# Kernel optimization log

Hardware: AMD Instinct MI355X
Metric: run time of the kernel (lower is better)

The kernel has to match this reference:

```python
import jax, jax.numpy as jnp
import numpy as np

N_NODES = 100_000
N_EDGES = 1_600_000
N_TRI = 1_000_000
HID = 64
NNZ0 = 2 * N_EDGES  # d0: 2 nonzeros per edge
NNZ1 = 3 * N_TRI    # d1: 3 nonzeros per 2-clique


def spmm(rows, cols, vals, x, n_out):
    """out[r] = sum_{k: rows[k]==r} vals[k] * x[cols[k]]  (sparse @ dense)."""
    return jax.ops.segment_sum(vals[:, None] * x[cols], rows, num_segments=n_out)


def setup_inputs() -> dict:
    key = jax.random.key(0)
    ks = jax.random.split(key, 12)
    q = jax.random.normal(ks[0], (N_NODES, HID), dtype=jnp.float32)
    p = jax.random.normal(ks[1], (N_EDGES, HID), dtype=jnp.float32)
    # attention weights used as divisors -> keep bounded away from 0
    A0 = jax.random.uniform(ks[2], (N_NODES,), jnp.float32, 0.5, 1.5)
    A1 = jax.random.uniform(ks[3], (N_EDGES,), jnp.float32, 0.5, 1.5)
    A2 = jax.random.uniform(ks[4], (N_TRI,), jnp.float32, 0.5, 1.5)
    alpha_raw = jnp.ones((1,), dtype=jnp.float32)
    d0_rows = jax.random.randint(ks[5], (NNZ0,), 0, N_EDGES, dtype=jnp.int32)
    d0_cols = jax.random.randint(ks[6], (NNZ0,), 0, N_NODES, dtype=jnp.int32)
    d0_vals = jax.random.normal(ks[7], (NNZ0,), dtype=jnp.float32)
    d1_rows = jax.random.randint(ks[8], (NNZ1,), 0, N_TRI, dtype=jnp.int32)
    d1_cols = jax.random.randint(ks[9], (NNZ1,), 0, N_EDGES, dtype=jnp.int32)
    d1_vals = jax.random.normal(ks[10], (NNZ1,), dtype=jnp.float32)
    return {
        "q": q, "p": p, "A0": A0, "A1": A1, "A2": A2, "alpha_raw": alpha_raw,
        "d0_rows": d0_rows, "d0_cols": d0_cols, "d0_vals": d0_vals,
        "d1_rows": d1_rows, "d1_cols": d1_cols, "d1_vals": d1_vals,
    }


def reference(q, p, A0, A1, A2, alpha_raw,
              d0_rows, d0_cols, d0_vals, d1_rows, d1_cols, d1_vals):
    n_nodes = q.shape[0]
    n_edges = p.shape[0]
    n_tri = A2.shape[0]
    alpha = jax.nn.sigmoid(alpha_raw)  # opt['alpha_multiplier']
    a0 = A0[:, None]  # [N,1]
    a1 = A1[:, None]  # [E,1]
    a2 = A2[:, None]  # [T,1]

    # bracket == 'gradient'
    # qPart = -alpha * d0^T (A1 * d0 (q / A0)) / A0
    d0ainvq = spmm(d0_rows, d0_cols, d0_vals, q / a0, n_edges)          # [E,H]
    qPart = -alpha * spmm(d0_cols, d0_rows, d0_vals, a1 * d0ainvq, n_nodes) / a0

    # pPart = -alpha * ( d1^T (A2 * d1 (p / A1)) / A1 + d0 (d0^T p / A0) )
    d1ainvp = spmm(d1_rows, d1_cols, d1_vals, p / a1, n_tri)            # [T,H]
    d1ad1Part = spmm(d1_cols, d1_rows, d1_vals, a2 * d1ainvp, n_edges) / a1
    a0invd0tp = spmm(d0_cols, d0_rows, d0_vals, p, n_nodes) / a0        # [N,H]
    d0d0aPart = spmm(d0_rows, d0_cols, d0_vals, a0invd0tp, n_edges)     # [E,H]
    pPart = -alpha * (d1ad1Part + d0d0aPart)

    return (qPart, pPart)
```

## Files before the change

kernel.cpp:

```cpp
#include <hip/hip_runtime.h>

#define HID 64

typedef unsigned short ushort_t;
typedef unsigned int uint_t;
typedef unsigned char uchar_t;
typedef unsigned long long ull_t;
typedef float fx4 __attribute__((ext_vector_type(4)));

__device__ __forceinline__ ushort_t f2bf(float f) {
    uint_t u = __float_as_uint(f);
    u += 0x7FFFu + ((u >> 16) & 1u);
    return (ushort_t)(u >> 16);
}
__device__ __forceinline__ float bf2f(ushort_t h) {
    return __uint_as_float(((uint_t)h) << 16);
}

__device__ __forceinline__ void ntstore4(float* dst, float a, float b, float c, float d) {
    fx4 t; t[0] = a; t[1] = b; t[2] = c; t[3] = d;
    __builtin_nontemporal_store(t, (fx4*)dst);
}

__device__ __forceinline__ int shard_of(int row, uint_t scale) {
    return (int)(((ull_t)(uint_t)row * scale) >> 32);
}


__global__ __launch_bounds__(256) void count_rank8(
    const int* __restrict__ d0r, const int* __restrict__ d0c,
    const int* __restrict__ d1r, const int* __restrict__ d1c,
    int* __restrict__ rowcat,
    uchar_t* __restrict__ rkA0, uchar_t* __restrict__ rkB0,
    uchar_t* __restrict__ rkA1, uchar_t* __restrict__ rkB1,
    int off_d0r, int off_d0c, int off_d1r, int off_d1c,
    int nnz0, int nnz1)
{
    int b = blockIdx.x;
    int cb0 = (nnz0 + 255) >> 8;
    if (b < cb0) {
        int k = b * 256 + threadIdx.x;
        if (k < nnz0) {
            int A = d0r[k], B = d0c[k];
            int r0 = atomicAdd(&rowcat[off_d0r + A + 1], 1);
            int r1 = atomicAdd(&rowcat[off_d0c + B + 1], 1);
            rkA0[k] = (uchar_t)r0;
            rkB0[k] = (uchar_t)r1;
        }
    } else {
        int k = (b - cb0) * 256 + threadIdx.x;
        if (k < nnz1) {
            int A = d1r[k], B = d1c[k];
            int r0 = atomicAdd(&rowcat[off_d1r + A + 1], 1);
            int r1 = atomicAdd(&rowcat[off_d1c + B + 1], 1);
            rkA1[k] = (uchar_t)r0;
            rkB1[k] = (uchar_t)r1;
        }
    }
}

__global__ __launch_bounds__(256) void fill_conv8(
    const int* __restrict__ d0r, const int* __restrict__ d0c,
    const float* __restrict__ v0, const float* __restrict__ A0d,
    const int* __restrict__ d1r, const int* __restrict__ d1c,
    const float* __restrict__ v1, const float* __restrict__ A1d,
    const int* __restrict__ S,
    const uchar_t* __restrict__ rkA0, const uchar_t* __restrict__ rkB0,
    const uchar_t* __restrict__ rkA1, const uchar_t* __restrict__ rkB1,
    int2* __restrict__ pcv,
    int off_d0r, int off_d0c, int off_d1r, int off_d1c,
    uint_t scE, uint_t scN, uint_t scT,
    int nnz0, int nnz1, int npair, int nchunks,
    const float* __restrict__ p, ushort_t* __restrict__ ph, long long np)
{
    int b = blockIdx.x;
    int shard = b & 7;
    int chunk = -1, vb = -1;
    int lim = 9 * npair;
    if (b < lim) {
        int g = b / 9, pos = b - g * 9;
        if (pos == 8) vb = g; else chunk = g;
    } else {
        int rem = b - lim;
        int fleft = (nchunks - npair) * 8;
        if (rem < fleft) chunk = npair + (rem >> 3);
        else vb = npair + (rem - fleft);
    }
    if (chunk >= 0) {
        int cb0 = (nnz0 + 255) >> 8;
        if (chunk < cb0) {
            int k = chunk * 256 + threadIdx.x;
            if (k < nnz0) {
                int A = d0r[k];
                int B = d0c[k];
                if (shard_of(A, scE) == shard) {
                    float v = v0[k];
                    int2 e; e.x = B; e.y = __float_as_int(v / A0d[B]);
                    pcv[S[off_d0r + A] + rkA0[k]] = e;
                }
                if (shard_of(B, scN) == shard) {
                    float v = v0[k];
                    int2 e; e.x = A; e.y = __float_as_int(v);
                    pcv[S[off_d0c + B] + rkB0[k]] = e;
                }
            }
        } else {
            int k = (chunk - cb0) * 256 + threadIdx.x;
            if (k < nnz1) {
                int A = d1r[k];
                int B = d1c[k];
                if (shard_of(A, scT) == shard) {
                    float v = v1[k];
                    int2 e; e.x = B; e.y = __float_as_int(v / A1d[B]);
                    pcv[S[off_d1r + A] + rkA1[k]] = e;
                }
                if (shard_of(B, scE) == shard) {
                    float v = v1[k];
                    int2 e; e.x = A; e.y = __float_as_int(v);
                    pcv[S[off_d1c + B] + rkB1[k]] = e;
                }
            }
        }
    } else if (vb >= 0) {
        const fx4* p4 = (const fx4*)p;
        ushort4* h4p = (ushort4*)ph;
        long long nf4 = np >> 2;
        long long f0 = (long long)vb * 1024 + threadIdx.x;
#pragma unroll
        for (int c = 0; c < 4; ++c) {
            long long f = f0 + c * 256;
            if (f < nf4) {
                fx4 v = __builtin_nontemporal_load(p4 + f);
                ushort4 o;
                o.x = f2bf(v[0]); o.y = f2bf(v[1]); o.z = f2bf(v[2]); o.w = f2bf(v[3]);
                h4p[f] = o;
            }
        }
    }
}

#define SCAN_TPB 256
#define SCAN_IPT 32
#define SCAN_TILE (SCAN_TPB * SCAN_IPT)

__global__ __launch_bounds__(256) void scan1(int* __restrict__ data,
                                             int* __restrict__ blockSums, int n) {
    __shared__ int sdata[SCAN_TPB];
    int base = blockIdx.x * SCAN_TILE + threadIdx.x * SCAN_IPT;
    int v[SCAN_IPT];
    int s = 0;
#pragma unroll
    for (int i = 0; i < SCAN_IPT; ++i) {
        int idx = base + i;
        int x = (idx < n) ? data[idx] : 0;
        s += x;
        v[i] = s;
    }
    sdata[threadIdx.x] = s;
    __syncthreads();
    for (int off = 1; off < SCAN_TPB; off <<= 1) {
        int t = (threadIdx.x >= off) ? sdata[threadIdx.x - off] : 0;
        __syncthreads();
        sdata[threadIdx.x] += t;
        __syncthreads();
    }
    int excl = (threadIdx.x == 0) ? 0 : sdata[threadIdx.x - 1];
#pragma unroll
    for (int i = 0; i < SCAN_IPT; ++i) {
        int idx = base + i;
        if (idx < n) data[idx] = v[i] + excl;
    }
    if (threadIdx.x == SCAN_TPB - 1) blockSums[blockIdx.x] = sdata[SCAN_TPB - 1];
}

__global__ __launch_bounds__(1024) void scan2(int* __restrict__ blockSums, int nb) {
    __shared__ int sdata[1024];
    int x = (threadIdx.x < nb) ? blockSums[threadIdx.x] : 0;
    sdata[threadIdx.x] = x;
    __syncthreads();
    for (int off = 1; off < 1024; off <<= 1) {
        int t = (threadIdx.x >= off) ? sdata[threadIdx.x - off] : 0;
        __syncthreads();
        sdata[threadIdx.x] += t;
        __syncthreads();
    }
    if (threadIdx.x < nb) blockSums[threadIdx.x] = sdata[threadIdx.x];
}

__global__ __launch_bounds__(256) void scan3(int* __restrict__ data,
                                             const int* __restrict__ blockSums, int n) {
    if (blockIdx.x == 0) return;
    int add = blockSums[blockIdx.x - 1];
    int base = blockIdx.x * SCAN_TILE + threadIdx.x;
#pragma unroll
    for (int i = 0; i < SCAN_IPT; ++i) {
        int idx = base + i * SCAN_TPB;
        if (idx < n) data[idx] += add;
    }
}


template <int SRCH>
__device__ __forceinline__ float4 gather_row(const void* __restrict__ xv, int col, int h4) {
    if constexpr (SRCH) {
        ushort4 hv = *((const ushort4*)((const ushort_t*)xv + (size_t)col * HID) + h4);
        float4 r; r.x = bf2f(hv.x); r.y = bf2f(hv.y); r.z = bf2f(hv.z); r.w = bf2f(hv.w);
        return r;
    } else {
        return *((const float4*)((const float*)xv + (size_t)col * HID) + h4);
    }
}

template <int SRCH, int OUTH>
__device__ __forceinline__ void spmm4_body(
    const int* __restrict__ rps, const int2* __restrict__ pcv,
    const void* __restrict__ xv, void* __restrict__ outv,
    const float* __restrict__ rmul, const float* __restrict__ rdiv,
    const float* __restrict__ alpha_raw, int nrows, int blk)
{
    int h4 = threadIdx.x & 15;
    int sub16 = threadIdx.x >> 4;
    int rbase = (blk * 16 + sub16) * 4;
    if (rbase >= nrows) return;
    int rp[5];
#pragma unroll
    for (int i = 0; i < 5; ++i) rp[i] = rps[min(rbase + i, nrows)];
    int len[4], last[4];
#pragma unroll
    for (int r = 0; r < 4; ++r) {
        len[r] = rp[r + 1] - rp[r];
        last[r] = max(rp[r + 1] - 1, 0);
    }
    int maxlen = max(max(len[0], len[1]), max(len[2], len[3]));
    float4 acc[4];
#pragma unroll
    for (int r = 0; r < 4; ++r) acc[r] = float4{0.f, 0.f, 0.f, 0.f};

    for (int j = 0; j < maxlen; j += 2) {
        int2 e0[4], e1[4];
#pragma unroll
        for (int r = 0; r < 4; ++r) {
            e0[r] = pcv[min(rp[r] + j, last[r])];
            e1[r] = pcv[min(rp[r] + j + 1, last[r])];
        }
        float4 g0[4], g1[4];
#pragma unroll
        for (int r = 0; r < 4; ++r) g0[r] = gather_row<SRCH>(xv, e0[r].x, h4);
#pragma unroll
        for (int r = 0; r < 4; ++r) g1[r] = gather_row<SRCH>(xv, e1[r].x, h4);
#pragma unroll
        for (int r = 0; r < 4; ++r) {
            float va = (j < len[r]) ? __int_as_float(e0[r].y) : 0.f;
            float vb = (j + 1 < len[r]) ? __int_as_float(e1[r].y) : 0.f;
            acc[r].x += va * g0[r].x + vb * g1[r].x;
            acc[r].y += va * g0[r].y + vb * g1[r].y;
            acc[r].z += va * g0[r].z + vb * g1[r].z;
            acc[r].w += va * g0[r].w + vb * g1[r].w;
        }
    }

    float sgn = alpha_raw ? -(1.0f / (1.0f + expf(-alpha_raw[0]))) : 1.0f;
#pragma unroll
    for (int r = 0; r < 4; ++r) {
        int row = rbase + r;
        if (row >= nrows) break;
        float s = sgn;
        if (rmul) s *= rmul[row];
        if (rdiv) s /= rdiv[row];
        float4 a = acc[r];
        a.x *= s; a.y *= s; a.z *= s; a.w *= s;
        if constexpr (OUTH) {
            ushort4 o;
            o.x = f2bf(a.x); o.y = f2bf(a.y); o.z = f2bf(a.z); o.w = f2bf(a.w);
            *((ushort4*)((ushort_t*)outv + (size_t)row * HID) + h4) = o;
        } else {
            ntstore4((float*)((float4*)((float*)outv + (size_t)row * HID) + h4),
                     a.x, a.y, a.z, a.w);
        }
    }
}

template <int SRCH, int OUTH>
__global__ __launch_bounds__(256) void csr_spmm4(
    const int* __restrict__ rps, const int2* __restrict__ pcv,
    const void* __restrict__ xv, void* __restrict__ outv,
    const float* __restrict__ rmul, const float* __restrict__ rdiv,
    const float* __restrict__ alpha_raw, int nrows)
{
    spmm4_body<SRCH, OUTH>(rps, pcv, xv, outv, rmul, rdiv, alpha_raw, nrows, blockIdx.x);
}

__global__ __launch_bounds__(256) void csr_spmm_dual(
    const int* __restrict__ rpsT, const int* __restrict__ rpsN,
    const int2* __restrict__ pcv, const ushort_t* __restrict__ ph,
    ushort_t* __restrict__ outT, ushort_t* __restrict__ outN,
    const float* __restrict__ a2, int n_tri, int n_nodes, int triBlocks)
{
    if ((int)blockIdx.x < triBlocks)
        spmm4_body<1, 1>(rpsT, pcv, ph, outT, a2, nullptr, nullptr, n_tri, blockIdx.x);
    else
        spmm4_body<1, 1>(rpsN, pcv, ph, outN, nullptr, nullptr, nullptr, n_nodes,
                         blockIdx.x - triBlocks);
}

__global__ __launch_bounds__(256) void csr_fused_epq(
    const int* __restrict__ rpsA, const int* __restrict__ rpsB,
    const int2* __restrict__ pcv,
    const float* __restrict__ q, const ushort_t* __restrict__ tmpn,
    const ushort_t* __restrict__ tmpt,
    const float* __restrict__ a1d, const float* __restrict__ alpha_raw,
    ushort_t* __restrict__ oute1, float* __restrict__ outp, int nrows)
{
    int h4 = threadIdx.x & 15;
    int sub16 = threadIdx.x >> 4;
    int rbase = (blockIdx.x * 16 + sub16) * 4;
    if (rbase >= nrows) return;

    int rpA[5], rpB[5];
#pragma unroll
    for (int i = 0; i < 5; ++i) {
        int idx = min(rbase + i, nrows);
        rpA[i] = rpsA[idx];
        rpB[i] = rpsB[idx];
    }
    int lA[4], lastA[4], lB[4], lastB[4];
#pragma unroll
    for (int r = 0; r < 4; ++r) {
        lA[r] = rpA[r + 1] - rpA[r]; lastA[r] = max(rpA[r + 1] - 1, 0);
        lB[r] = rpB[r + 1] - rpB[r]; lastB[r] = max(rpB[r + 1] - 1, 0);
    }
    int mA = max(max(lA[0], lA[1]), max(lA[2], lA[3]));
    int mB = max(max(lB[0], lB[1]), max(lB[2], lB[3]));

    float4 accQ[4], accN[4], accT[4];
#pragma unroll
    for (int r = 0; r < 4; ++r) {
        accQ[r] = float4{0.f, 0.f, 0.f, 0.f};
        accN[r] = float4{0.f, 0.f, 0.f, 0.f};
        accT[r] = float4{0.f, 0.f, 0.f, 0.f};
    }

    for (int j = 0; j < mA; ++j) {
        int2 e[4];
#pragma unroll
        for (int r = 0; r < 4; ++r) e[r] = pcv[min(rpA[r] + j, lastA[r])];
        float4 gq[4]; ushort4 gn[4];
#pragma unroll
        for (int r = 0; r < 4; ++r)
            gq[r] = *((const float4*)(q + (size_t)e[r].x * HID) + h4);
#pragma unroll
        for (int r = 0; r < 4; ++r)
            gn[r] = *((const ushort4*)(tmpn + (size_t)e[r].x * HID) + h4);
#pragma unroll
        for (int r = 0; r < 4; ++r) {
            float v = (j < lA[r]) ? __int_as_float(e[r].y) : 0.f;
            accQ[r].x += v * gq[r].x; accQ[r].y += v * gq[r].y;
            accQ[r].z += v * gq[r].z; accQ[r].w += v * gq[r].w;
            accN[r].x += v * bf2f(gn[r].x); accN[r].y += v * bf2f(gn[r].y);
            accN[r].z += v * bf2f(gn[r].z); accN[r].w += v * bf2f(gn[r].w);
        }
    }

    for (int j = 0; j < mB; j += 2) {
        int2 e0[4], e1[4];
#pragma unroll
        for (int r = 0; r < 4; ++r) {
            e0[r] = pcv[min(rpB[r] + j, lastB[r])];
            e1[r] = pcv[min(rpB[r] + j + 1, lastB[r])];
        }
        ushort4 g0[4], g1[4];
#pragma unroll
        for (int r = 0; r < 4; ++r)
            g0[r] = *((const ushort4*)(tmpt + (size_t)e0[r].x * HID) + h4);
#pragma unroll
        for (int r = 0; r < 4; ++r)
            g1[r] = *((const ushort4*)(tmpt + (size_t)e1[r].x * HID) + h4);
#pragma unroll
        for (int r = 0; r < 4; ++r) {
            float va = (j < lB[r]) ? __int_as_float(e0[r].y) : 0.f;
            float vb = (j + 1 < lB[r]) ? __int_as_float(e1[r].y) : 0.f;
            accT[r].x += va * bf2f(g0[r].x) + vb * bf2f(g1[r].x);
            accT[r].y += va * bf2f(g0[r].y) + vb * bf2f(g1[r].y);
            accT[r].z += va * bf2f(g0[r].z) + vb * bf2f(g1[r].z);
            accT[r].w += va * bf2f(g0[r].w) + vb * bf2f(g1[r].w);
        }
    }

    float ns = -(1.0f / (1.0f + expf(-alpha_raw[0])));
#pragma unroll
    for (int r = 0; r < 4; ++r) {
        int row = rbase + r;
        if (row >= nrows) break;
        float a1v = a1d[row];
        ushort4 o;
        o.x = f2bf(accQ[r].x * a1v); o.y = f2bf(accQ[r].y * a1v);
        o.z = f2bf(accQ[r].z * a1v); o.w = f2bf(accQ[r].w * a1v);
        *((ushort4*)(oute1 + (size_t)row * HID) + h4) = o;
        float ia = 1.0f / a1v;
        ntstore4((float*)((float4*)(outp + (size_t)row * HID) + h4),
                 ns * (accN[r].x + accT[r].x * ia),
                 ns * (accN[r].y + accT[r].y * ia),
                 ns * (accN[r].z + accT[r].z * ia),
                 ns * (accN[r].w + accT[r].w * ia));
    }
}


__global__ __launch_bounds__(256) void count_rows(const int* __restrict__ ridx,
                                                  int* __restrict__ rowptr, int nnz) {
    int k = blockIdx.x * 256 + threadIdx.x;
    if (k < nnz) atomicAdd(&rowptr[ridx[k] + 1], 1);
}

__global__ __launch_bounds__(256) void copy_int(const int* __restrict__ src,
                                                int* __restrict__ dst, int n) {
    int i = blockIdx.x * 256 + threadIdx.x;
    if (i < n) dst[i] = src[i];
}

__global__ __launch_bounds__(256) void fill_csr(const int* __restrict__ ridx,
                                                const int* __restrict__ cidx,
                                                const float* __restrict__ vals,
                                                int* __restrict__ cursor,
                                                int2* __restrict__ pcv, int nnz) {
    int k = blockIdx.x * 256 + threadIdx.x;
    if (k >= nnz) return;
    int pos = atomicAdd(&cursor[ridx[k]], 1);
    int2 e;
    e.x = cidx[k];
    e.y = __float_as_int(vals[k]);
    pcv[pos] = e;
}

template <int SRCH, int OUTH>
__global__ __launch_bounds__(256) void csr_spmm_t(
    const int* __restrict__ rowptr, const int2* __restrict__ pcv,
    const void* __restrict__ xv, void* __restrict__ outv,
    const float* __restrict__ gdiag, int gdiv,
    const float* __restrict__ rmul,
    const float* __restrict__ rdiv,
    const float* __restrict__ alpha_raw,
    int nrows)
{
    int lane = threadIdx.x & 63;
    int wave = threadIdx.x >> 6;
    int sub = lane >> 4;
    int h4 = lane & 15;
    int row = blockIdx.x * 16 + wave * 4 + sub;
    if (row >= nrows) return;
    int start = rowptr[row], end = rowptr[row + 1];
    float4 acc = {0.f, 0.f, 0.f, 0.f};
    for (int j = start; j < end; ++j) {
        int2 e = pcv[j];
        int c = e.x;
        float v = __int_as_float(e.y);
        if (gdiag) { float t = gdiag[c]; v = gdiv ? v / t : v * t; }
        float4 xvv = gather_row<SRCH>(xv, c, h4);
        acc.x += v * xvv.x; acc.y += v * xvv.y; acc.z += v * xvv.z; acc.w += v * xvv.w;
    }
    float s = 1.0f;
    if (rmul) s *= rmul[row];
    if (rdiv) s /= rdiv[row];
    if (alpha_raw) s *= -(1.0f / (1.0f + expf(-alpha_raw[0])));
    acc.x *= s; acc.y *= s; acc.z *= s; acc.w *= s;
    if constexpr (OUTH) {
        ushort_t* out = (ushort_t*)outv;
        ushort4 o;
        o.x = f2bf(acc.x); o.y = f2bf(acc.y); o.z = f2bf(acc.z); o.w = f2bf(acc.w);
        *((ushort4*)(out + (size_t)row * HID) + h4) = o;
    } else {
        float* out = (float*)outv;
        *((float4*)(out + (size_t)row * HID) + h4) = acc;
    }
}

template <int BH>
__global__ __launch_bounds__(256) void csr_spmm_fused_t(
    const int* __restrict__ rowptrA, const int2* __restrict__ pcvA, const float* __restrict__ xA,
    const int* __restrict__ rowptrB, const int2* __restrict__ pcvB, const void* __restrict__ xBv,
    const float* __restrict__ a1, const float* __restrict__ alpha_raw,
    float* __restrict__ out, int nrows)
{
    int lane = threadIdx.x & 63;
    int wave = threadIdx.x >> 6;
    int sub = lane >> 4;
    int h4 = lane & 15;
    int row = blockIdx.x * 16 + wave * 4 + sub;
    if (row >= nrows) return;

    float4 accA = {0.f, 0.f, 0.f, 0.f};
    {
        int start = rowptrA[row], end = rowptrA[row + 1];
        for (int j = start; j < end; ++j) {
            int2 e = pcvA[j];
            float v = __int_as_float(e.y);
            const float4 xv = *((const float4*)(xA + (size_t)e.x * HID) + h4);
            accA.x += v * xv.x; accA.y += v * xv.y; accA.z += v * xv.z; accA.w += v * xv.w;
        }
    }
    float4 accB = {0.f, 0.f, 0.f, 0.f};
    {
        int start = rowptrB[row], end = rowptrB[row + 1];
        for (int j = start; j < end; ++j) {
            int2 e = pcvB[j];
            float v = __int_as_float(e.y);
            float4 xv = gather_row<BH>(xBv, e.x, h4);
            accB.x += v * xv.x; accB.y += v * xv.y; accB.z += v * xv.z; accB.w += v * xv.w;
        }
    }
    float inv_a1 = 1.0f / a1[row];
    float ns = -(1.0f / (1.0f + expf(-alpha_raw[0])));
    float4 r;
    r.x = ns * (accA.x + accB.x * inv_a1);
    r.y = ns * (accA.y + accB.y * inv_a1);
    r.z = ns * (accA.z + accB.z * inv_a1);
    r.w = ns * (accA.w + accB.w * inv_a1);
    *((float4*)(out + (size_t)row * HID) + h4) = r;
}

__global__ __launch_bounds__(256) void spmm_scatter(
    const int* __restrict__ gidx, const int* __restrict__ sidx,
    const float* __restrict__ vals, const float* __restrict__ x,
    float* __restrict__ out,
    const float* __restrict__ gscale, int ginv,
    const float* __restrict__ sscale, int sinv,
    const float* __restrict__ alpha_raw, int nnz)
{
    int k = (blockIdx.x << 2) | (threadIdx.x >> 6);
    if (k >= nnz) return;
    int h = threadIdx.x & 63;
    int g = gidx[k];
    int s = sidx[k];
    float f = vals[k];
    if (gscale) { float t = gscale[g]; f = ginv ? (f / t) : (f * t); }
    if (sscale) { float t = sscale[s]; f = sinv ? (f / t) : (f * t); }
    if (alpha_raw) {
        float sig = 1.0f / (1.0f + expf(-alpha_raw[0]));
        f = -f * sig;
    }
    atomicAdd(out + (size_t)s * HID + h, f * x[(size_t)g * HID + h]);
}


extern "C" void kernel_launch(void* const* d_in, const int* in_sizes, int n_in,
                              void* d_out, int out_size, void* d_ws, size_t ws_size,
                              hipStream_t stream) {
    const float* q         = (const float*)d_in[0];
    const float* p         = (const float*)d_in[1];
    const float* A0        = (const float*)d_in[2];
    const float* A1        = (const float*)d_in[3];
    const float* A2        = (const float*)d_in[4];
    const float* alpha_raw = (const float*)d_in[5];
    const int*   d0_rows   = (const int*)d_in[6];
    const int*   d0_cols   = (const int*)d_in[7];
    const float* d0_vals   = (const float*)d_in[8];
    const int*   d1_rows   = (const int*)d_in[9];
    const int*   d1_cols   = (const int*)d_in[10];
    const float* d1_vals   = (const float*)d_in[11];

    const int n_nodes = in_sizes[2];
    const int n_edges = in_sizes[3];
    const int n_tri   = in_sizes[4];
    const int nnz0    = in_sizes[6];
    const int nnz1    = in_sizes[9];

    float* qPart = (float*)d_out;
    float* pPart = (float*)d_out + (size_t)n_nodes * HID;

    const size_t qPartBytes = (size_t)n_nodes * HID * sizeof(float);
    const size_t pPartBytes = (size_t)n_edges * HID * sizeof(float);

    dim3 blk(256);

    const int off_d0r = 0;
    const int off_d0c = off_d0r + n_edges;
    const int off_d1r = off_d0c + n_nodes;
    const int off_d1c = off_d1r + n_tri;
    const int NR      = off_d1c + n_edges;

    {
        char* w = (char*)d_ws;
        auto alloc = [&](size_t bytes) -> char* {
            char* ptr = w;
            w += (bytes + 255) & ~(size_t)255;
            return ptr;
        };
        ushort_t* bufA   = (ushort_t*)alloc((size_t)n_edges * HID * sizeof(ushort_t));
        ushort_t* tmp_th = (ushort_t*)alloc((size_t)n_tri * HID * sizeof(ushort_t));
        ushort_t* tmp_nh = (ushort_t*)alloc((size_t)n_nodes * HID * sizeof(ushort_t));
        int*      Z      = (int*)alloc((size_t)(NR + 2) * sizeof(int));
        int*      S      = Z + 1;
        int*      blockSums = (int*)alloc(2048 * sizeof(int));
        int2*     pcvcat = (int2*)alloc(((size_t)nnz0 * 2 + (size_t)nnz1 * 2) * sizeof(int2));
        size_t rankBytes = 2 * ((size_t)nnz0 + (size_t)nnz1);
        uchar_t* rkA0;
        if (rankBytes <= (size_t)n_tri * HID * sizeof(ushort_t))
            rkA0 = (uchar_t*)tmp_th;
        else
            rkA0 = (uchar_t*)alloc(rankBytes);
        uchar_t* rkB0 = rkA0 + nnz0;
        uchar_t* rkA1 = rkB0 + nnz0;
        uchar_t* rkB1 = rkA1 + nnz1;
        size_t needed = (size_t)(w - (char*)d_ws);

        if (needed <= ws_size) {
            hipMemsetAsync(Z, 0, (size_t)(NR + 2) * sizeof(int), stream);
            int cb0 = (nnz0 + 255) / 256;
            int cb1 = (nnz1 + 255) / 256;
            count_rank8<<<cb0 + cb1, blk, 0, stream>>>(
                d0_rows, d0_cols, d1_rows, d1_cols, S,
                rkA0, rkB0, rkA1, rkB1,
                off_d0r, off_d0c, off_d1r, off_d1c, nnz0, nnz1);
            {
                int n = NR + 1;
                int nb = (n + SCAN_TILE - 1) / SCAN_TILE;
                scan1<<<nb, SCAN_TPB, 0, stream>>>(S, blockSums, n);
                scan2<<<1, 1024, 0, stream>>>(blockSums, nb);
                scan3<<<nb, SCAN_TPB, 0, stream>>>(S, blockSums, n);
            }
            long long np = (long long)n_edges * HID;
            int cbc = (int)((np / 4 + 1023) / 1024);
            int nchunks = cb0 + cb1;
            int npair = min(nchunks, cbc);
            int grid = 9 * npair + 8 * (nchunks - npair) + (cbc - npair);
            auto mksc = [](int n) -> uint_t {
                return (uint_t)(((unsigned long long)8 << 32) / (unsigned)n);
            };
            fill_conv8<<<grid, blk, 0, stream>>>(
                d0_rows, d0_cols, d0_vals, A0,
                d1_rows, d1_cols, d1_vals, A1,
                S, rkA0, rkB0, rkA1, rkB1, pcvcat,
                off_d0r, off_d0c, off_d1r, off_d1c,
                mksc(n_edges), mksc(n_nodes), mksc(n_tri),
                nnz0, nnz1, npair, nchunks,
                p, bufA, np);

            int triB  = (n_tri + 63) / 64;
            int nodeB = (n_nodes + 63) / 64;
            int edgeB = (n_edges + 63) / 64;

            csr_spmm_dual<<<triB + nodeB, blk, 0, stream>>>(
                S + off_d1r, S + off_d0c, pcvcat, bufA, tmp_th, tmp_nh,
                A2, n_tri, n_nodes, triB);

            csr_fused_epq<<<edgeB, blk, 0, stream>>>(
                S + off_d0r, S + off_d1c, pcvcat, q, tmp_nh, tmp_th,
                A1, alpha_raw, bufA, pPart, n_edges);

            csr_spmm4<1, 0><<<nodeB, blk, 0, stream>>>(
                S + off_d0c, pcvcat, bufA, qPart, nullptr, A0, alpha_raw, n_nodes);
            return;
        }
    }

    {
        char* w = (char*)d_ws;
        auto alloc = [&](size_t bytes) -> char* {
            char* ptr = w;
            w += (bytes + 255) & ~(size_t)255;
            return ptr;
        };
        float* tmp_t = (float*)alloc((size_t)n_tri * HID * sizeof(float));
        float* tmp_n = (float*)alloc((size_t)n_nodes * HID * sizeof(float));
        size_t rpTotal = (size_t)(n_edges + 1) + (n_nodes + 1) + (n_tri + 1) + (n_edges + 1);
        int* rpBase = (int*)alloc(rpTotal * sizeof(int));
        int* rp_d0r = rpBase;
        int* rp_d0c = rp_d0r + (n_edges + 1);
        int* rp_d1r = rp_d0c + (n_nodes + 1);
        int* rp_d1c = rp_d1r + (n_tri + 1);
        int nmax = n_edges > n_tri ? n_edges : n_tri;
        if (n_nodes > nmax) nmax = n_nodes;
        int* cursor    = (int*)alloc((size_t)nmax * sizeof(int));
        int* blockSums = (int*)alloc(2048 * sizeof(int));
        int2* pcv_d0r = (int2*)alloc((size_t)nnz0 * sizeof(int2));
        int2* pcv_d0c = (int2*)alloc((size_t)nnz0 * sizeof(int2));
        int2* pcv_d1r = (int2*)alloc((size_t)nnz1 * sizeof(int2));
        int2* pcv_d1c = (int2*)alloc((size_t)nnz1 * sizeof(int2));
        size_t needed = (size_t)(w - (char*)d_ws);

        if (needed <= ws_size) {
            hipMemsetAsync(rpBase, 0, rpTotal * sizeof(int), stream);
            dim3 gk0((nnz0 + 255) / 256);
            dim3 gk1((nnz1 + 255) / 256);
            count_rows<<<gk0, blk, 0, stream>>>(d0_rows, rp_d0r, nnz0);
            count_rows<<<gk0, blk, 0, stream>>>(d0_cols, rp_d0c, nnz0);
            count_rows<<<gk1, blk, 0, stream>>>(d1_rows, rp_d1r, nnz1);
            count_rows<<<gk1, blk, 0, stream>>>(d1_cols, rp_d1c, nnz1);

            struct Build {
                int* rowptr; int nout; const int* ridx; const int* cidx; const float* vals;
                int2* pcv; int nnz;
            } builds[4] = {
                { rp_d0r, n_edges, d0_rows, d0_cols, d0_vals, pcv_d0r, nnz0 },
                { rp_d0c, n_nodes, d0_cols, d0_rows, d0_vals, pcv_d0c, nnz0 },
                { rp_d1r, n_tri,   d1_rows, d1_cols, d1_vals, pcv_d1r, nnz1 },
                { rp_d1c, n_edges, d1_cols, d1_rows, d1_vals, pcv_d1c, nnz1 },
            };
            for (int b = 0; b < 4; ++b) {
                int n = builds[b].nout + 1;
                int nb = (n + SCAN_TILE - 1) / SCAN_TILE;
                scan1<<<nb, SCAN_TPB, 0, stream>>>(builds[b].rowptr, blockSums, n);
                scan2<<<1, 1024, 0, stream>>>(blockSums, nb);
                scan3<<<nb, SCAN_TPB, 0, stream>>>(builds[b].rowptr, blockSums, n);
                copy_int<<<(builds[b].nout + 255) / 256, blk, 0, stream>>>(
                    builds[b].rowptr, cursor, builds[b].nout);
                fill_csr<<<(builds[b].nnz + 255) / 256, blk, 0, stream>>>(
                    builds[b].ridx, builds[b].cidx, builds[b].vals, cursor,
                    builds[b].pcv, builds[b].nnz);
            }

            float* tmp_e1 = pPart;
            csr_spmm_t<0, 0><<<(n_edges + 15) / 16, blk, 0, stream>>>(
                rp_d0r, pcv_d0r, q, tmp_e1, A0, 1, A1, nullptr, nullptr, n_edges);
            csr_spmm_t<0, 0><<<(n_nodes + 15) / 16, blk, 0, stream>>>(
                rp_d0c, pcv_d0c, tmp_e1, qPart, nullptr, 0, nullptr, A0, alpha_raw, n_nodes);
            csr_spmm_t<0, 0><<<(n_tri + 15) / 16, blk, 0, stream>>>(
                rp_d1r, pcv_d1r, p, tmp_t, A1, 1, A2, nullptr, nullptr, n_tri);
            csr_spmm_t<0, 0><<<(n_nodes + 15) / 16, blk, 0, stream>>>(
                rp_d0c, pcv_d0c, p, tmp_n, nullptr, 0, nullptr, A0, nullptr, n_nodes);
            csr_spmm_fused_t<0><<<(n_edges + 15) / 16, blk, 0, stream>>>(
                rp_d0r, pcv_d0r, tmp_n,
                rp_d1c, pcv_d1c, tmp_t,
                A1, alpha_raw, pPart, n_edges);
            return;
        }
    }

    {
        float* tmp = (float*)d_ws;
        const size_t triBytes  = (size_t)n_tri * HID * sizeof(float);
        const size_t nodeBytes = qPartBytes;
        dim3 g0((nnz0 + 3) / 4);
        dim3 g1((nnz1 + 3) / 4);
        hipMemsetAsync(qPart, 0, qPartBytes, stream);
        hipMemsetAsync(pPart, 0, pPartBytes, stream);
        spmm_scatter<<<g0, blk, 0, stream>>>(d0_cols, d0_rows, d0_vals, q, pPart,
                                             A0, 1, nullptr, 0, nullptr, nnz0);
        spmm_scatter<<<g0, blk, 0, stream>>>(d0_rows, d0_cols, d0_vals, pPart, qPart,
                                             A1, 0, A0, 1, alpha_raw, nnz0);
        hipMemsetAsync(pPart, 0, pPartBytes, stream);
        hipMemsetAsync(tmp, 0, triBytes, stream);
        spmm_scatter<<<g1, blk, 0, stream>>>(d1_cols, d1_rows, d1_vals, p, tmp,
                                             A1, 1, nullptr, 0, nullptr, nnz1);
        spmm_scatter<<<g1, blk, 0, stream>>>(d1_rows, d1_cols, d1_vals, tmp, pPart,
                                             A2, 0, A1, 1, alpha_raw, nnz1);
        hipMemsetAsync(tmp, 0, nodeBytes, stream);
        spmm_scatter<<<g0, blk, 0, stream>>>(d0_rows, d0_cols, d0_vals, p, tmp,
                                             nullptr, 0, A0, 1, nullptr, nnz0);
        spmm_scatter<<<g0, blk, 0, stream>>>(d0_cols, d0_rows, d0_vals, tmp, pPart,
                                             nullptr, 0, nullptr, 0, alpha_raw, nnz0);
    }
}
```

Before: 1.923 ms.

## Fuse CSR build phases into a single cooperative kernel with grid syncs

```diff
diff --git a/kernel.cpp b/kernel.cpp
--- a/kernel.cpp
+++ b/kernel.cpp
@@ -1,6 +1,11 @@
 #include <hip/hip_runtime.h>
+#include <hip/hip_cooperative_groups.h>
+
+namespace cg = cooperative_groups;
 
 #define HID 64
+#define BT 24
+#define BUILD_BLOCKS 1024
 
 typedef unsigned short ushort_t;
 typedef unsigned int uint_t;
@@ -22,10 +27,169 @@
     __builtin_nontemporal_store(t, (fx4*)dst);
 }
 
+#define SCAN_TPB 256
+#define SCAN_IPT 32
+#define SCAN_TILE (SCAN_TPB * SCAN_IPT)
+
+
+__global__ __launch_bounds__(256, 4) void build_all(
+    const int* __restrict__ d0r, const int* __restrict__ d0c,
+    const float* __restrict__ v0, const float* __restrict__ A0d,
+    const int* __restrict__ d1r, const int* __restrict__ d1c,
+    const float* __restrict__ v1, const float* __restrict__ A1d,
+    int* __restrict__ Z,
+    int* __restrict__ blockSums,
+    int2* __restrict__ pcv,
+    int off_d0r, int off_d0c, int off_d1r, int off_d1c,
+    int nnz0, int nnz1, int NR,
+    const float* __restrict__ p, ushort_t* __restrict__ ph, long long np)
+{
+    cg::grid_group grid = cg::this_grid();
+    const int nth = gridDim.x * 256;
+    const int tid = blockIdx.x * 256 + threadIdx.x;
+    int* S = Z + 1;
+    const int E = nnz0 + nnz1;
+    const fx4* p4 = (const fx4*)p;
+    ushort4* h4p = (ushort4*)ph;
+    const long long nf4 = np >> 2;
+    const long long nf4h = nf4 >> 1;
+
+    for (int i = tid; i < NR + 2; i += nth) Z[i] = 0;
+    __threadfence();
+    grid.sync();
+
+    uint_t rk[BT];
+#pragma unroll
+    for (int i = 0; i < BT; ++i) {
+        int k = tid + i * nth;
+        uint_t r = 0;
+        if (k < nnz0) {
+            int A = d0r[k], B = d0c[k];
+            uint_t ra = (uint_t)atomicAdd(&S[off_d0r + A + 1], 1);
+            uint_t rb = (uint_t)atomicAdd(&S[off_d0c + B + 1], 1);
+            r = (ra << 16) | rb;
+        } else if (k < E) {
+            int kk = k - nnz0;
+            int A = d1r[kk], B = d1c[kk];
+            uint_t ra = (uint_t)atomicAdd(&S[off_d1r + A + 1], 1);
+            uint_t rb = (uint_t)atomicAdd(&S[off_d1c + B + 1], 1);
+            r = (ra << 16) | rb;
+        }
+        rk[i] = r;
+    }
+    for (long long f = tid; f < nf4h; f += nth) {
+        fx4 v = __builtin_nontemporal_load(p4 + f);
+        ushort4 o;
+        o.x = f2bf(v[0]); o.y = f2bf(v[1]); o.z = f2bf(v[2]); o.w = f2bf(v[3]);
+        h4p[f] = o;
+    }
+    __threadfence();
+    grid.sync();
+
+    const int n = NR + 1;
+    const int ntiles = (n + SCAN_TILE - 1) / SCAN_TILE;
+    __shared__ int sdata[SCAN_TPB];
+    if ((int)blockIdx.x < ntiles) {
+        int base = blockIdx.x * SCAN_TILE + threadIdx.x * SCAN_IPT;
+        int v[SCAN_IPT];
+        int s = 0;
+#pragma unroll
+        for (int i = 0; i < SCAN_IPT; ++i) {
+            int idx = base + i;
+            int x = (idx < n) ? S[idx] : 0;
+            s += x;
+            v[i] = s;
+        }
+        sdata[threadIdx.x] = s;
+        __syncthreads();
+        for (int off = 1; off < SCAN_TPB; off <<= 1) {
+            int t = (threadIdx.x >= off) ? sdata[threadIdx.x - off] : 0;
+            __syncthreads();
+            sdata[threadIdx.x] += t;
+            __syncthreads();
+        }
+        int excl = (threadIdx.x == 0) ? 0 : sdata[threadIdx.x - 1];
+#pragma unroll
+        for (int i = 0; i < SCAN_IPT; ++i) {
+            int idx = base + i;
+            if (idx < n) S[idx] = v[i] + excl;
+        }
+        if (threadIdx.x == SCAN_TPB - 1) blockSums[blockIdx.x] = sdata[SCAN_TPB - 1];
+    }
+    __threadfence();
+    grid.sync();
+    if (blockIdx.x == 0) {
+        int vv[8];
+        int acc = 0;
+#pragma unroll
+        for (int i = 0; i < 8; ++i) {
+            int idx = threadIdx.x * 8 + i;
+            int x = (idx < ntiles) ? blockSums[idx] : 0;
+            acc += x;
+            vv[i] = acc;
+        }
+        sdata[threadIdx.x] = acc;
+        __syncthreads();
+        for (int off = 1; off < SCAN_TPB; off <<= 1) {
+            int t = (threadIdx.x >= off) ? sdata[threadIdx.x - off] : 0;
+            __syncthreads();
+            sdata[threadIdx.x] += t;
+            __syncthreads();
+        }
+        int excl = (threadIdx.x == 0) ? 0 : sdata[threadIdx.x - 1];
+#pragma unroll
+        for (int i = 0; i < 8; ++i) {
+            int idx = threadIdx.x * 8 + i;
+            if (idx < ntiles) blockSums[idx] = vv[i] + excl;
+        }
+    }
+    __threadfence();
+    grid.sync();
+    if (blockIdx.x >= 1 && (int)blockIdx.x < ntiles) {
+        int add = blockSums[blockIdx.x - 1];
+        int base = blockIdx.x * SCAN_TILE + threadIdx.x;
+#pragma unroll
+        for (int i = 0; i < SCAN_IPT; ++i) {
+            int idx = base + i * SCAN_TPB;
+            if (idx < n) S[idx] += add;
+        }
+    }
+    __threadfence();
+    grid.sync();
+
+#pragma unroll
+    for (int i = 0; i < BT; ++i) {
+        int k = tid + i * nth;
+        uint_t r = rk[i];
+        if (k < nnz0) {
+            int A = d0r[k], B = d0c[k];
+            float v = v0[k];
+            int2 ea; ea.x = B; ea.y = __float_as_int(v / A0d[B]);
+            pcv[S[off_d0r + A] + (int)(r >> 16)] = ea;
+            int2 eb; eb.x = A; eb.y = __float_as_int(v);
+            pcv[S[off_d0c + B] + (int)(r & 0xFFFFu)] = eb;
+        } else if (k < E) {
+            int kk = k - nnz0;
+            int A = d1r[kk], B = d1c[kk];
+            float v = v1[kk];
+            int2 ea; ea.x = B; ea.y = __float_as_int(v / A1d[B]);
+            pcv[S[off_d1r + A] + (int)(r >> 16)] = ea;
+            int2 eb; eb.x = A; eb.y = __float_as_int(v);
+            pcv[S[off_d1c + B] + (int)(r & 0xFFFFu)] = eb;
+        }
+    }
+    for (long long f = nf4h + tid; f < nf4; f += nth) {
+        fx4 v = __builtin_nontemporal_load(p4 + f);
+        ushort4 o;
+        o.x = f2bf(v[0]); o.y = f2bf(v[1]); o.z = f2bf(v[2]); o.w = f2bf(v[3]);
+        h4p[f] = o;
+    }
+}
+
+
 __device__ __forceinline__ int shard_of(int row, uint_t scale) {
     return (int)(((ull_t)(uint_t)row * scale) >> 32);
 }
-
 
 __global__ __launch_bounds__(256) void count_rank8(
     const int* __restrict__ d0r, const int* __restrict__ d0c,
@@ -139,10 +303,6 @@
     }
 }
 
-#define SCAN_TPB 256
-#define SCAN_IPT 32
-#define SCAN_TILE (SCAN_TPB * SCAN_IPT)
-
 __global__ __launch_bounds__(256) void scan1(int* __restrict__ data,
                                              int* __restrict__ blockSums, int n) {
     __shared__ int sdata[SCAN_TPB];
@@ -604,36 +764,69 @@
         size_t needed = (size_t)(w - (char*)d_ws);
 
         if (needed <= ws_size) {
-            hipMemsetAsync(Z, 0, (size_t)(NR + 2) * sizeof(int), stream);
-            int cb0 = (nnz0 + 255) / 256;
-            int cb1 = (nnz1 + 255) / 256;
-            count_rank8<<<cb0 + cb1, blk, 0, stream>>>(
-                d0_rows, d0_cols, d1_rows, d1_cols, S,
-                rkA0, rkB0, rkA1, rkB1,
-                off_d0r, off_d0c, off_d1r, off_d1c, nnz0, nnz1);
+            long long np = (long long)n_edges * HID;
+            long long E = (long long)nnz0 + nnz1;
+            int ntiles = (NR + 1 + SCAN_TILE - 1) / SCAN_TILE;
+
+            bool coop_done = false;
             {
-                int n = NR + 1;
-                int nb = (n + SCAN_TILE - 1) / SCAN_TILE;
-                scan1<<<nb, SCAN_TPB, 0, stream>>>(S, blockSums, n);
-                scan2<<<1, 1024, 0, stream>>>(blockSums, nb);
-                scan3<<<nb, SCAN_TPB, 0, stream>>>(S, blockSums, n);
+                static int coop_support = -1;
+                if (coop_support < 0) {
+                    int dev = 0, v = 0;
+                    if (hipGetDevice(&dev) == hipSuccess)
+                        if (hipDeviceGetAttribute(&v, hipDeviceAttributeCooperativeLaunch,
+                                                  dev) != hipSuccess)
+                            v = 0;
+                    coop_support = v;
+                }
+                bool fits = (E <= (long long)BT * BUILD_BLOCKS * 256) && (ntiles <= 2048);
+                if (coop_support > 0 && fits) {
+                    void* ka[] = {
+                        (void*)&d0_rows, (void*)&d0_cols, (void*)&d0_vals, (void*)&A0,
+                        (void*)&d1_rows, (void*)&d1_cols, (void*)&d1_vals, (void*)&A1,
+                        (void*)&Z, (void*)&blockSums, (void*)&pcvcat,
+                        (void*)&off_d0r, (void*)&off_d0c, (void*)&off_d1r, (void*)&off_d1c,
+                        (void*)&nnz0, (void*)&nnz1, (void*)&NR,
+                        (void*)&p, (void*)&bufA, (void*)&np
+                    };
+                    hipError_t err = hipLaunchCooperativeKernel(
+                        (const void*)build_all, dim3(BUILD_BLOCKS), dim3(256),
+                        ka, 0, stream);
+                    coop_done = (err == hipSuccess);
+                }
             }
-            long long np = (long long)n_edges * HID;
-            int cbc = (int)((np / 4 + 1023) / 1024);
-            int nchunks = cb0 + cb1;
-            int npair = min(nchunks, cbc);
-            int grid = 9 * npair + 8 * (nchunks - npair) + (cbc - npair);
-            auto mksc = [](int n) -> uint_t {
-                return (uint_t)(((unsigned long long)8 << 32) / (unsigned)n);
-            };
-            fill_conv8<<<grid, blk, 0, stream>>>(
-                d0_rows, d0_cols, d0_vals, A0,
-                d1_rows, d1_cols, d1_vals, A1,
-                S, rkA0, rkB0, rkA1, rkB1, pcvcat,
-                off_d0r, off_d0c, off_d1r, off_d1c,
-                mksc(n_edges), mksc(n_nodes), mksc(n_tri),
-                nnz0, nnz1, npair, nchunks,
-                p, bufA, np);
+
+            if (!coop_done) {
+                hipMemsetAsync(Z, 0, (size_t)(NR + 2) * sizeof(int), stream);
+                int cb0 = (nnz0 + 255) / 256;
+                int cb1 = (nnz1 + 255) / 256;
+                count_rank8<<<cb0 + cb1, blk, 0, stream>>>(
+                    d0_rows, d0_cols, d1_rows, d1_cols, S,
+                    rkA0, rkB0, rkA1, rkB1,
+                    off_d0r, off_d0c, off_d1r, off_d1c, nnz0, nnz1);
+                {
+                    int n = NR + 1;
+                    int nb = (n + SCAN_TILE - 1) / SCAN_TILE;
+                    scan1<<<nb, SCAN_TPB, 0, stream>>>(S, blockSums, n);
+                    scan2<<<1, 1024, 0, stream>>>(blockSums, nb);
+                    scan3<<<nb, SCAN_TPB, 0, stream>>>(S, blockSums, n);
+                }
+                int cbc = (int)((np / 4 + 1023) / 1024);
+                int nchunks = cb0 + cb1;
+                int npair = min(nchunks, cbc);
+                int grid = 9 * npair + 8 * (nchunks - npair) + (cbc - npair);
+                auto mksc = [](int n) -> uint_t {
+                    return (uint_t)(((unsigned long long)8 << 32) / (unsigned)n);
+                };
+                fill_conv8<<<grid, blk, 0, stream>>>(
+                    d0_rows, d0_cols, d0_vals, A0,
+                    d1_rows, d1_cols, d1_vals, A1,
+                    S, rkA0, rkB0, rkA1, rkB1, pcvcat,
+                    off_d0r, off_d0c, off_d1r, off_d1c,
+                    mksc(n_edges), mksc(n_nodes), mksc(n_tri),
+                    nnz0, nnz1, npair, nchunks,
+                    p, bufA, np);
+            }
 
             int triB  = (n_tri + 63) / 64;
             int nodeB = (n_nodes + 63) / 64;
```

Result: slower. 2.931 ms (+52.4%).

## Gather q as bf16 in fused edge kernel and deepen SpMM unrolling

Applied to the files above, without the earlier changes.

```diff
diff --git a/kernel.cpp b/kernel.cpp
--- a/kernel.cpp
+++ b/kernel.cpp
@@ -27,17 +27,19 @@
 }
 
 
-__global__ __launch_bounds__(256) void count_rank8(
+__global__ __launch_bounds__(256) void count_rank_convq(
     const int* __restrict__ d0r, const int* __restrict__ d0c,
     const int* __restrict__ d1r, const int* __restrict__ d1c,
     int* __restrict__ rowcat,
     uchar_t* __restrict__ rkA0, uchar_t* __restrict__ rkB0,
     uchar_t* __restrict__ rkA1, uchar_t* __restrict__ rkB1,
     int off_d0r, int off_d0c, int off_d1r, int off_d1c,
-    int nnz0, int nnz1)
+    int nnz0, int nnz1,
+    const float* __restrict__ q, ushort_t* __restrict__ qh, long long nq)
 {
     int b = blockIdx.x;
     int cb0 = (nnz0 + 255) >> 8;
+    int cb1 = (nnz1 + 255) >> 8;
     if (b < cb0) {
         int k = b * 256 + threadIdx.x;
         if (k < nnz0) {
@@ -47,7 +49,7 @@
             rkA0[k] = (uchar_t)r0;
             rkB0[k] = (uchar_t)r1;
         }
-    } else {
+    } else if (b < cb0 + cb1) {
         int k = (b - cb0) * 256 + threadIdx.x;
         if (k < nnz1) {
             int A = d1r[k], B = d1c[k];
@@ -55,6 +57,22 @@
             int r1 = atomicAdd(&rowcat[off_d1c + B + 1], 1);
             rkA1[k] = (uchar_t)r0;
             rkB1[k] = (uchar_t)r1;
+        }
+    } else {
+        int vb = b - cb0 - cb1;
+        const fx4* q4 = (const fx4*)q;
+        ushort4* h4p = (ushort4*)qh;
+        long long nf4 = nq >> 2;
+        long long f0 = (long long)vb * 1024 + threadIdx.x;
+#pragma unroll
+        for (int c = 0; c < 4; ++c) {
+            long long f = f0 + c * 256;
+            if (f < nf4) {
+                fx4 v = __builtin_nontemporal_load(q4 + f);
+                ushort4 o;
+                o.x = f2bf(v[0]); o.y = f2bf(v[1]); o.z = f2bf(v[2]); o.w = f2bf(v[3]);
+                h4p[f] = o;
+            }
         }
     }
 }
@@ -236,27 +254,29 @@
 #pragma unroll
     for (int r = 0; r < 4; ++r) acc[r] = float4{0.f, 0.f, 0.f, 0.f};
 
-    for (int j = 0; j < maxlen; j += 2) {
-        int2 e0[4], e1[4];
-#pragma unroll
-        for (int r = 0; r < 4; ++r) {
-            e0[r] = pcv[min(rp[r] + j, last[r])];
-            e1[r] = pcv[min(rp[r] + j + 1, last[r])];
-        }
-        float4 g0[4], g1[4];
-#pragma unroll
-        for (int r = 0; r < 4; ++r) g0[r] = gather_row<SRCH>(xv, e0[r].x, h4);
-#pragma unroll
-        for (int r = 0; r < 4; ++r) g1[r] = gather_row<SRCH>(xv, e1[r].x, h4);
-#pragma unroll
-        for (int r = 0; r < 4; ++r) {
-            float va = (j < len[r]) ? __int_as_float(e0[r].y) : 0.f;
-            float vb = (j + 1 < len[r]) ? __int_as_float(e1[r].y) : 0.f;
-            acc[r].x += va * g0[r].x + vb * g1[r].x;
-            acc[r].y += va * g0[r].y + vb * g1[r].y;
-            acc[r].z += va * g0[r].z + vb * g1[r].z;
-            acc[r].w += va * g0[r].w + vb * g1[r].w;
-        }
+    for (int j = 0; j < maxlen; j += 4) {
+        int2 e[4][4];
+#pragma unroll
+        for (int u = 0; u < 4; ++u)
+#pragma unroll
+            for (int r = 0; r < 4; ++r)
+                e[u][r] = pcv[min(rp[r] + j + u, last[r])];
+        float4 g[4][4];
+#pragma unroll
+        for (int u = 0; u < 4; ++u)
+#pragma unroll
+            for (int r = 0; r < 4; ++r)
+                g[u][r] = gather_row<SRCH>(xv, e[u][r].x, h4);
+#pragma unroll
+        for (int u = 0; u < 4; ++u)
+#pragma unroll
+            for (int r = 0; r < 4; ++r) {
+                float v = (j + u < len[r]) ? __int_as_float(e[u][r].y) : 0.f;
+                acc[r].x += v * g[u][r].x;
+                acc[r].y += v * g[u][r].y;
+                acc[r].z += v * g[u][r].z;
+                acc[r].w += v * g[u][r].w;
+            }
     }
 
     float sgn = alpha_raw ? -(1.0f / (1.0f + expf(-alpha_raw[0]))) : 1.0f;
@@ -306,7 +326,7 @@
 __global__ __launch_bounds__(256) void csr_fused_epq(
     const int* __restrict__ rpsA, const int* __restrict__ rpsB,
     const int2* __restrict__ pcv,
-    const float* __restrict__ q, const ushort_t* __restrict__ tmpn,
+    const ushort_t* __restrict__ qh, const ushort_t* __restrict__ tmpn,
     const ushort_t* __restrict__ tmpt,
     const float* __restrict__ a1d, const float* __restrict__ alpha_raw,
     ushort_t* __restrict__ oute1, float* __restrict__ outp, int nrows)
@@ -340,24 +360,36 @@
         accT[r] = float4{0.f, 0.f, 0.f, 0.f};
     }
 
-    for (int j = 0; j < mA; ++j) {
-        int2 e[4];
-#pragma unroll
-        for (int r = 0; r < 4; ++r) e[r] = pcv[min(rpA[r] + j, lastA[r])];
-        float4 gq[4]; ushort4 gn[4];
-#pragma unroll
-        for (int r = 0; r < 4; ++r)
-            gq[r] = *((const float4*)(q + (size_t)e[r].x * HID) + h4);
-#pragma unroll
-        for (int r = 0; r < 4; ++r)
-            gn[r] = *((const ushort4*)(tmpn + (size_t)e[r].x * HID) + h4);
+    for (int j = 0; j < mA; j += 2) {
+        int2 e0[4], e1[4];
 #pragma unroll
         for (int r = 0; r < 4; ++r) {
-            float v = (j < lA[r]) ? __int_as_float(e[r].y) : 0.f;
-            accQ[r].x += v * gq[r].x; accQ[r].y += v * gq[r].y;
-            accQ[r].z += v * gq[r].z; accQ[r].w += v * gq[r].w;
-            accN[r].x += v * bf2f(gn[r].x); accN[r].y += v * bf2f(gn[r].y);
-            accN[r].z += v * bf2f(gn[r].z); accN[r].w += v * bf2f(gn[r].w);
+            e0[r] = pcv[min(rpA[r] + j, lastA[r])];
+            e1[r] = pcv[min(rpA[r] + j + 1, lastA[r])];
+        }
+        ushort4 gq0[4], gq1[4], gn0[4], gn1[4];
+#pragma unroll
+        for (int r = 0; r < 4; ++r) {
+            gq0[r] = *((const ushort4*)(qh + (size_t)e0[r].x * HID) + h4);
+            gn0[r] = *((const ushort4*)(tmpn + (size_t)e0[r].x * HID) + h4);
+        }
+#pragma unroll
+        for (int r = 0; r < 4; ++r) {
+            gq1[r] = *((const ushort4*)(qh + (size_t)e1[r].x * HID) + h4);
+            gn1[r] = *((const ushort4*)(tmpn + (size_t)e1[r].x * HID) + h4);
+        }
+#pragma unroll
+        for (int r = 0; r < 4; ++r) {
+            float va = (j < lA[r]) ? __int_as_float(e0[r].y) : 0.f;
+            float vb = (j + 1 < lA[r]) ? __int_as_float(e1[r].y) : 0.f;
+            accQ[r].x += va * bf2f(gq0[r].x) + vb * bf2f(gq1[r].x);
+            accQ[r].y += va * bf2f(gq0[r].y) + vb * bf2f(gq1[r].y);
+            accQ[r].z += va * bf2f(gq0[r].z) + vb * bf2f(gq1[r].z);
+            accQ[r].w += va * bf2f(gq0[r].w) + vb * bf2f(gq1[r].w);
+            accN[r].x += va * bf2f(gn0[r].x) + vb * bf2f(gn1[r].x);
+            accN[r].y += va * bf2f(gn0[r].y) + vb * bf2f(gn1[r].y);
+            accN[r].z += va * bf2f(gn0[r].z) + vb * bf2f(gn1[r].z);
+            accN[r].w += va * bf2f(gn0[r].w) + vb * bf2f(gn1[r].w);
         }
     }
 
@@ -588,6 +620,7 @@
         ushort_t* bufA   = (ushort_t*)alloc((size_t)n_edges * HID * sizeof(ushort_t));
         ushort_t* tmp_th = (ushort_t*)alloc((size_t)n_tri * HID * sizeof(ushort_t));
         ushort_t* tmp_nh = (ushort_t*)alloc((size_t)n_nodes * HID * sizeof(ushort_t));
+        ushort_t* q_h    = (ushort_t*)alloc((size_t)n_nodes * HID * sizeof(ushort_t));
         int*      Z      = (int*)alloc((size_t)(NR + 2) * sizeof(int));
         int*      S      = Z + 1;
         int*      blockSums = (int*)alloc(2048 * sizeof(int));
@@ -607,10 +640,13 @@
             hipMemsetAsync(Z, 0, (size_t)(NR + 2) * sizeof(int), stream);
             int cb0 = (nnz0 + 255) / 256;
             int cb1 = (nnz1 + 255) / 256;
-            count_rank8<<<cb0 + cb1, blk, 0, stream>>>(
+            long long nq = (long long)n_nodes * HID;
+            int qcb = (int)((nq / 4 + 1023) / 1024);
+            count_rank_convq<<<cb0 + cb1 + qcb, blk, 0, stream>>>(
                 d0_rows, d0_cols, d1_rows, d1_cols, S,
                 rkA0, rkB0, rkA1, rkB1,
-                off_d0r, off_d0c, off_d1r, off_d1c, nnz0, nnz1);
+                off_d0r, off_d0c, off_d1r, off_d1c, nnz0, nnz1,
+                q, q_h, nq);
             {
                 int n = NR + 1;
                 int nb = (n + SCAN_TILE - 1) / SCAN_TILE;
@@ -644,7 +680,7 @@
                 A2, n_tri, n_nodes, triB);
 
             csr_fused_epq<<<edgeB, blk, 0, stream>>>(
-                S + off_d0r, S + off_d1c, pcvcat, q, tmp_nh, tmp_th,
+                S + off_d0r, S + off_d1c, pcvcat, q_h, tmp_nh, tmp_th,
                 A1, alpha_raw, bufA, pPart, n_edges);
 
             csr_spmm4<1, 0><<<nodeB, blk, 0, stream>>>(
```

Result: slower. 1.963 ms (+2.1%).
